# Optimization experiments

Hardware: AMD Instinct MI355X
Metric: run time of the kernel (lower is better)

Reference implementation:

```python
import jax, jax.numpy as jnp
import numpy as np


def setup_inputs() -> dict:
    key = jax.random.key(0)
    B, D, H, W = 4, 2, 2048, 2048
    # displacement field in voxels (B, D, H, W); ~1 voxel displacements
    phi = jax.random.normal(key, (B, D, H, W), dtype=jnp.float32)
    return {"phi": phi}


def reference(phi):
    """Count/splat ones through a displacement field with bilinear weights
    and 'wrap' (periodic) boundary conditions.

    phi : (B, 2, H, W) displacement in voxels -> count : (B, 1, H, W)
    """
    B, D, H, W = phi.shape
    ii = jnp.arange(H, dtype=phi.dtype)[:, None]   # (H,1)
    jj = jnp.arange(W, dtype=phi.dtype)[None, :]   # (1,W)
    # sample positions = identity + displacement
    x = ii + phi[:, 0]                             # (B,H,W) along dim 0
    y = jj + phi[:, 1]                             # (B,H,W) along dim 1

    x0 = jnp.floor(x)
    y0 = jnp.floor(y)
    wx1 = x - x0                                   # fractional weights
    wy1 = y - y0
    wx0 = 1.0 - wx1
    wy0 = 1.0 - wy1

    # periodic (wrap) boundary: indices mod size
    ix0 = jnp.mod(x0.astype(jnp.int32), H)
    ix1 = jnp.mod(ix0 + 1, H)
    iy0 = jnp.mod(y0.astype(jnp.int32), W)
    iy1 = jnp.mod(iy0 + 1, W)

    boff = (jnp.arange(B, dtype=jnp.int32) * (H * W))[:, None, None]  # batch offset

    out = jnp.zeros((B * H * W,), dtype=phi.dtype)

    def splat(acc, ix, iy, w):
        idx = (boff + ix * W + iy).ravel()
        return acc.at[idx].add(w.ravel())

    out = splat(out, ix0, iy0, wx0 * wy0)
    out = splat(out, ix0, iy1, wx0 * wy1)
    out = splat(out, ix1, iy0, wx1 * wy0)
    out = splat(out, ix1, iy1, wx1 * wy1)

    return out.reshape(B, 1, H, W)
```

## Files before the change

kernel.cpp:

```cpp
#include <hip/hip_runtime.h>

constexpr int H = 2048, W = 2048;
constexpr int HW = H * W;
constexpr int OUTW = 56;
constexpr int NCH = (W + OUTW - 1) / OUTW;
constexpr int RB  = 4;
constexpr int WPB = 4;
constexpr int ROWSPB = RB * WPB;
constexpr int NSRC = RB + 6;

__global__ __launch_bounds__(256)
void splat_gather4f(const float* __restrict__ phi, float* __restrict__ out,
                    unsigned char* __restrict__ flags) {
    int wid  = threadIdx.x >> 6;
    int lane = threadIdx.x & 63;

    const int rgPerImg = H / ROWSPB;
    int bid = blockIdx.x;
    int b   = bid / (NCH * rgPerImg);
    int rem = bid - b * (NCH * rgPerImg);
    int c0i = rem / rgPerImg;
    int rg  = rem - c0i * rgPerImg;
    int r0  = rg * ROWSPB + wid * RB;
    int c0  = c0i * OUTW;

    const float* phiB = phi + (size_t)b * 2 * HW;
    float* outb = out + (size_t)b * HW;

    int scu = c0 - 4 + lane;
    int scw = scu & (W - 1);
    bool ownedCol = (lane >= 4) && (lane < 4 + OUTW) && (scu < W);

    float dxv[NSRC], dyv[NSRC];
    #pragma unroll
    for (int t = 0; t < NSRC; ++t) {
        int srow = (r0 + t - 3) & (H - 1);
        dxv[t] = phiB[(size_t)srow * W + scw];
        dyv[t] = phiB[(size_t)HW + (size_t)srow * W + scw];
    }

    float slot[RB][7];
    #pragma unroll
    for (int m = 0; m < RB; ++m)
        #pragma unroll
        for (int k = 0; k < 7; ++k) slot[m][k] = 0.0f;

    #pragma unroll
    for (int t = 0; t < NSRC; ++t) {
        float dx = dxv[t], dy = dyv[t];
        bool valid = (__builtin_fabsf(dx) < 3.0f) && (__builtin_fabsf(dy) < 3.0f);
        float dyM = valid ? dy : 16384.0f;

        float ct[7];
        #pragma unroll
        for (int k = 0; k < 7; ++k) {
            float d = dyM - (float)(k - 3);
            ct[k] = __builtin_fmaxf(1.0f - __builtin_fabsf(d), 0.0f);
        }

        #pragma unroll
        for (int m = 0; m < RB; ++m) {
            if (t - m < 0 || t - m > 6) continue;
            float dist = dx + (float)(t - 3 - m);
            float rw = __builtin_fmaxf(1.0f - __builtin_fabsf(dist), 0.0f);
            #pragma unroll
            for (int k = 0; k < 7; ++k)
                slot[m][k] = __builtin_fmaf(rw, ct[k], slot[m][k]);
        }

        if (t >= 3 && t < 3 + RB) {
            bool need = (!valid) && ownedCol;
            unsigned long long mask = __ballot(need);
            if (lane == 0) {
                int srow = (r0 + t - 3) & (H - 1);
                flags[(size_t)(b * H + srow) * NCH + c0i] = (mask != 0ull) ? 1 : 0;
            }
        }
    }

    #pragma unroll
    for (int m = 0; m < RB; ++m) {
        float v = 0.0f;
        #pragma unroll
        for (int k = 0; k < 7; ++k)
            v += __shfl(slot[m][k], lane - (k - 3));
        if (ownedCol)
            outb[(size_t)(r0 + m) * W + scu] = v;
    }
}

__global__ __launch_bounds__(256)
void flush_flagged(const float* __restrict__ phi, const unsigned char* __restrict__ flags,
                   float* __restrict__ out) {
    int wid  = threadIdx.x >> 6;
    int lane = threadIdx.x & 63;
    long long chunk = (long long)blockIdx.x * WPB + wid;

    if (!flags[chunk]) return;

    int c0i = (int)(chunk % NCH);
    long long bs = chunk / NCH;
    int srow = (int)(bs & (H - 1));
    int b    = (int)(bs >> 11);

    int col = c0i * OUTW + lane;
    if (lane >= OUTW || col >= W) return;

    const float* phiB = phi + (size_t)b * 2 * HW;
    float dx = phiB[(size_t)srow * W + col];
    float dy = phiB[(size_t)HW + (size_t)srow * W + col];
    if ((__builtin_fabsf(dx) < 3.0f) && (__builtin_fabsf(dy) < 3.0f)) return;

    float* outb = out + (size_t)b * HW;
    float x = (float)srow + dx;
    float y = (float)col + dy;
    float x0 = floorf(x), y0 = floorf(y);
    float wx1 = x - x0, wx0 = 1.0f - wx1;
    float wy1 = y - y0, wy0 = 1.0f - wy1;
    int gx0 = ((int)x0) & (H - 1);
    int gx1 = (gx0 + 1) & (H - 1);
    int gy0 = ((int)y0) & (W - 1);
    int gy1 = (gy0 + 1) & (W - 1);
    atomicAdd(outb + (size_t)gx0 * W + gy0, wx0 * wy0);
    atomicAdd(outb + (size_t)gx0 * W + gy1, wx0 * wy1);
    atomicAdd(outb + (size_t)gx1 * W + gy0, wx1 * wy0);
    atomicAdd(outb + (size_t)gx1 * W + gy1, wx1 * wy1);
}

extern "C" void kernel_launch(void* const* d_in, const int* in_sizes, int n_in,
                              void* d_out, int out_size, void* d_ws, size_t ws_size,
                              hipStream_t stream) {
    const float* phi = (const float*)d_in[0];
    float* out = (float*)d_out;
    unsigned char* flags = (unsigned char*)d_ws;

    int B = out_size / HW;
    int grid = B * NCH * (H / ROWSPB);
    splat_gather4f<<<grid, 256, 0, stream>>>(phi, out, flags);

    long long nChunks = (long long)B * H * NCH;
    int grid2 = (int)(nChunks / WPB);
    flush_flagged<<<grid2, 256, 0, stream>>>(phi, flags, out);
}
```

Measured before the change: 94.04 us.

## Pack tent-weight FMAs into float2 and batch flag scanning in flush kernel

The gather kernel's per-tap tent weights and slot accumulations now use two-wide float vectors. This lets the compiler emit packed FP32 FMA/max instructions and roughly halve the VALU instruction count of the inner loop. The flush kernel now has each wave read 64 flags at once and ballot them, then loop only over set flags. That shrinks its grid by 64x and removes the launch and scheduling cost of tens of thousands of mostly-empty blocks. In exchange, flagged chunks are handled serially within a wave, and the 7-tap accumulation carries one unused packed lane.

```diff
diff --git a/kernel.cpp b/kernel.cpp
--- a/kernel.cpp
+++ b/kernel.cpp
@@ -9,8 +9,16 @@
 constexpr int ROWSPB = RB * WPB;
 constexpr int NSRC = RB + 6;
 
+typedef float f32x2 __attribute__((ext_vector_type(2)));
+
+__device__ __forceinline__ f32x2 pk_tent(f32x2 d) {
+    f32x2 a = __builtin_elementwise_max(d, -d);
+    f32x2 t = (f32x2)(1.0f) - a;
+    return __builtin_elementwise_max(t, (f32x2)(0.0f));
+}
+
 __global__ __launch_bounds__(256)
-void splat_gather4f(const float* __restrict__ phi, float* __restrict__ out,
+void splat_gather4p(const float* __restrict__ phi, float* __restrict__ out,
                     unsigned char* __restrict__ flags) {
     int wid  = threadIdx.x >> 6;
     int lane = threadIdx.x & 63;
@@ -39,11 +47,11 @@
         dyv[t] = phiB[(size_t)HW + (size_t)srow * W + scw];
     }
 
-    float slot[RB][7];
+    f32x2 slot[RB][4];
     #pragma unroll
     for (int m = 0; m < RB; ++m)
         #pragma unroll
-        for (int k = 0; k < 7; ++k) slot[m][k] = 0.0f;
+        for (int p = 0; p < 4; ++p) slot[m][p] = (f32x2)(0.0f);
 
     #pragma unroll
     for (int t = 0; t < NSRC; ++t) {
@@ -51,11 +59,12 @@
         bool valid = (__builtin_fabsf(dx) < 3.0f) && (__builtin_fabsf(dy) < 3.0f);
         float dyM = valid ? dy : 16384.0f;
 
-        float ct[7];
+        f32x2 dy2 = {dyM, dyM};
+        f32x2 ct[4];
         #pragma unroll
-        for (int k = 0; k < 7; ++k) {
-            float d = dyM - (float)(k - 3);
-            ct[k] = __builtin_fmaxf(1.0f - __builtin_fabsf(d), 0.0f);
+        for (int p = 0; p < 4; ++p) {
+            const f32x2 koff = {(float)(2 * p - 3), (float)(2 * p - 2)};
+            ct[p] = pk_tent(dy2 - koff);
         }
 
         #pragma unroll
@@ -63,9 +72,10 @@
             if (t - m < 0 || t - m > 6) continue;
             float dist = dx + (float)(t - 3 - m);
             float rw = __builtin_fmaxf(1.0f - __builtin_fabsf(dist), 0.0f);
+            f32x2 rw2 = {rw, rw};
             #pragma unroll
-            for (int k = 0; k < 7; ++k)
-                slot[m][k] = __builtin_fmaf(rw, ct[k], slot[m][k]);
+            for (int p = 0; p < 4; ++p)
+                slot[m][p] = __builtin_elementwise_fma(rw2, ct[p], slot[m][p]);
         }
 
         if (t >= 3 && t < 3 + RB) {
@@ -82,8 +92,11 @@
     for (int m = 0; m < RB; ++m) {
         float v = 0.0f;
         #pragma unroll
-        for (int k = 0; k < 7; ++k)
-            v += __shfl(slot[m][k], lane - (k - 3));
+        for (int p = 0; p < 4; ++p) {
+            v += __shfl(slot[m][p].x, lane - (2 * p - 3));
+            if (p < 3)
+                v += __shfl(slot[m][p].y, lane - (2 * p - 2));
+        }
         if (ownedCol)
             outb[(size_t)(r0 + m) * W + scu] = v;
     }
@@ -94,37 +107,44 @@
                    float* __restrict__ out) {
     int wid  = threadIdx.x >> 6;
     int lane = threadIdx.x & 63;
-    long long chunk = (long long)blockIdx.x * WPB + wid;
+    unsigned base = ((unsigned)blockIdx.x * WPB + (unsigned)wid) * 64u;
 
-    if (!flags[chunk]) return;
+    unsigned char f = flags[base + (unsigned)lane];
+    unsigned long long mask = __ballot(f != 0);
 
-    int c0i = (int)(chunk % NCH);
-    long long bs = chunk / NCH;
-    int srow = (int)(bs & (H - 1));
-    int b    = (int)(bs >> 11);
+    while (mask) {
+        int bit = (int)(__ffsll((long long)mask) - 1);
+        mask &= mask - 1ull;
+        unsigned chunk = base + (unsigned)bit;
 
-    int col = c0i * OUTW + lane;
-    if (lane >= OUTW || col >= W) return;
+        int c0i  = (int)(chunk % (unsigned)NCH);
+        unsigned bs = chunk / (unsigned)NCH;
+        int srow = (int)(bs & (H - 1));
+        int b    = (int)(bs >> 11);
 
-    const float* phiB = phi + (size_t)b * 2 * HW;
-    float dx = phiB[(size_t)srow * W + col];
-    float dy = phiB[(size_t)HW + (size_t)srow * W + col];
-    if ((__builtin_fabsf(dx) < 3.0f) && (__builtin_fabsf(dy) < 3.0f)) return;
-
-    float* outb = out + (size_t)b * HW;
-    float x = (float)srow + dx;
-    float y = (float)col + dy;
-    float x0 = floorf(x), y0 = floorf(y);
-    float wx1 = x - x0, wx0 = 1.0f - wx1;
-    float wy1 = y - y0, wy0 = 1.0f - wy1;
-    int gx0 = ((int)x0) & (H - 1);
-    int gx1 = (gx0 + 1) & (H - 1);
-    int gy0 = ((int)y0) & (W - 1);
-    int gy1 = (gy0 + 1) & (W - 1);
-    atomicAdd(outb + (size_t)gx0 * W + gy0, wx0 * wy0);
-    atomicAdd(outb + (size_t)gx0 * W + gy1, wx0 * wy1);
-    atomicAdd(outb + (size_t)gx1 * W + gy0, wx1 * wy0);
-    atomicAdd(outb + (size_t)gx1 * W + gy1, wx1 * wy1);
+        int col = c0i * OUTW + lane;
+        if (lane < OUTW && col < W) {
+            const float* phiB = phi + (size_t)b * 2 * HW;
+            float dx = phiB[(size_t)srow * W + col];
+            float dy = phiB[(size_t)HW + (size_t)srow * W + col];
+            if (!((__builtin_fabsf(dx) < 3.0f) && (__builtin_fabsf(dy) < 3.0f))) {
+                float* outb = out + (size_t)b * HW;
+                float x = (float)srow + dx;
+                float y = (float)col + dy;
+                float x0 = floorf(x), y0 = floorf(y);
+                float wx1 = x - x0, wx0 = 1.0f - wx1;
+                float wy1 = y - y0, wy0 = 1.0f - wy1;
+                int gx0 = ((int)x0) & (H - 1);
+                int gx1 = (gx0 + 1) & (H - 1);
+                int gy0 = ((int)y0) & (W - 1);
+                int gy1 = (gy0 + 1) & (W - 1);
+                atomicAdd(outb + (size_t)gx0 * W + gy0, wx0 * wy0);
+                atomicAdd(outb + (size_t)gx0 * W + gy1, wx0 * wy1);
+                atomicAdd(outb + (size_t)gx1 * W + gy0, wx1 * wy0);
+                atomicAdd(outb + (size_t)gx1 * W + gy1, wx1 * wy1);
+            }
+        }
+    }
 }
 
 extern "C" void kernel_launch(void* const* d_in, const int* in_sizes, int n_in,
@@ -136,9 +156,9 @@
 
     int B = out_size / HW;
     int grid = B * NCH * (H / ROWSPB);
-    splat_gather4f<<<grid, 256, 0, stream>>>(phi, out, flags);
+    splat_gather4p<<<grid, 256, 0, stream>>>(phi, out, flags);
 
     long long nChunks = (long long)B * H * NCH;
-    int grid2 = (int)(nChunks / WPB);
+    int grid2 = (int)(nChunks / (WPB * 64));
     flush_flagged<<<grid2, 256, 0, stream>>>(phi, flags, out);
 }
```

After: 100.6 us. 6.9% more time.
